# Kernel optimization log

Hardware: AMD Instinct MI355X
Metric: run time of the kernel (lower is better)

## Reference

```python
import jax, jax.numpy as jnp
import numpy as np

B = 16
NS = [2048, 1024, 512, 256]
K = 12
GROUPS = 64
OUT = 1024
EPS = 1e-5


def setup_inputs() -> dict:
    key = jax.random.key(0)
    ks = iter(jax.random.split(key, 40))
    d = {}
    for i, n in enumerate(NS):
        d[f"fs{i}"] = jax.random.normal(next(ks), (B, n, 256), jnp.float32)
        d[f"xs{i}"] = jax.random.normal(next(ks), (B, n, 3), jnp.float32)
        ct = 1024 if i == 0 else 256
        d[f"ft{i}"] = jax.random.normal(next(ks), (B, n, ct), jnp.float32)
        d[f"xt{i}"] = jax.random.normal(next(ks), (B, n, 3), jnp.float32)
    d["Ws"] = jax.random.normal(next(ks), (4, OUT, 256), jnp.float32) * 0.05
    d["bWs"] = jax.random.normal(next(ks), (4, OUT), jnp.float32) * 0.05
    d["gs"] = jax.random.uniform(next(ks), (4, OUT), jnp.float32, 0.5, 1.5)
    d["bes"] = jax.random.normal(next(ks), (4, OUT), jnp.float32) * 0.05
    d["mus"] = jax.random.normal(next(ks), (4, OUT), jnp.float32) * 0.05
    d["vs"] = jax.random.uniform(next(ks), (4, OUT), jnp.float32, 0.5, 1.5)
    d["Wt0"] = jax.random.normal(next(ks), (OUT, 1024), jnp.float32) * 0.02
    d["Wt123"] = jax.random.normal(next(ks), (3, OUT, 256), jnp.float32) * 0.05
    d["bWt"] = jax.random.normal(next(ks), (4, OUT), jnp.float32) * 0.05
    d["gt"] = jax.random.uniform(next(ks), (4, OUT), jnp.float32, 0.5, 1.5)
    d["bet"] = jax.random.normal(next(ks), (4, OUT), jnp.float32) * 0.05
    d["mut"] = jax.random.normal(next(ks), (4, OUT), jnp.float32) * 0.05
    d["vt"] = jax.random.uniform(next(ks), (4, OUT), jnp.float32, 0.5, 1.5)
    return d


def fps(xyz, m):
    # furthest point sampling starting from index 0 (as in pointnet2_utils)
    b, n, _ = xyz.shape
    idxs = jnp.zeros((b, m), jnp.int32)
    d2 = jnp.full((b, n), 1e10, xyz.dtype)
    last = jnp.zeros((b,), jnp.int32)

    def body(i, st):
        idxs, d2, last = st
        lx = jnp.take_along_axis(xyz, last[:, None, None], axis=1)  # [b,1,3]
        d = jnp.sum((xyz - lx) ** 2, axis=-1)  # [b,n]
        d2 = jnp.minimum(d2, d)
        nxt = jnp.argmax(d2, axis=-1).astype(jnp.int32)
        return idxs.at[:, i].set(nxt), d2, nxt

    idxs, _, _ = jax.lax.fori_loop(1, m, body, (idxs, d2, last))
    return idxs


def gather_points(feat, idx):
    # feat [b,n,c], idx [b,...] -> [b,...,c]
    flat = idx.reshape(idx.shape[0], -1)
    out = jnp.take_along_axis(feat, flat[..., None], axis=1)
    return out.reshape(idx.shape + (feat.shape[-1],))


def knn_point(k, xyz, query):
    # squared pairwise distances [b,m,n]; k smallest (== torch.topk largest=False)
    d = (jnp.sum(query ** 2, -1, keepdims=True)
         - 2.0 * jnp.einsum('bmd,bnd->bmn', query, xyz)
         + jnp.sum(xyz ** 2, -1)[:, None, :])
    _, idx = jax.lax.top_k(-d, k)
    return idx.astype(jnp.int32)


def graph_op(grouped, w, b, g, be, mu, v):
    # grouped [B,M,K,C]; kernel-1 Conv1d == channel matmul; eval-mode BN; ReLU; max over K
    x = jnp.einsum('bmkc,oc->bmko', grouped, w) + b
    x = (x - mu) * (g * jax.lax.rsqrt(v + EPS)) + be
    x = jax.nn.relu(x)
    return jnp.max(x, axis=2)  # [B,M,O]


def reference(fs0, xs0, ft0, xt0, fs1, xs1, ft1, xt1, fs2, xs2, ft2, xt2,
              fs3, xs3, ft3, xt3, Ws, bWs, gs, bes, mus, vs,
              Wt0, Wt123, bWt, gt, bet, mut, vt):
    fs_list = [fs0, fs1, fs2, fs3]
    xs_list = [xs0, xs1, xs2, xs3]
    ft_list = [ft0, ft1, ft2, ft3]
    xt_list = [xt0, xt1, xt2, xt3]

    fps_idx = fps(xt_list[-1], GROUPS)              # [B,G]
    new_xyz = gather_points(xt_list[-1], fps_idx)   # [B,G,3]

    out_s, out_t = [], []
    for i in range(4):
        idx_t = knn_point(K, xt_list[i], new_xyz)   # [B,G,K]
        grp_t = gather_points(ft_list[i], idx_t)    # [B,G,K,Ct]
        idx_s = knn_point(K, xs_list[i], new_xyz)
        grp_s = gather_points(fs_list[i], idx_s)    # [B,G,K,256]
        wt = Wt0 if i == 0 else Wt123[i - 1]
        out_s.append(graph_op(grp_s, Ws[i], bWs[i], gs[i], bes[i], mus[i], vs[i]))
        out_t.append(graph_op(grp_t, wt, bWt[i], gt[i], bet[i], mut[i], vt[i]))
    return (tuple(out_s), tuple(out_t))
```

## Files before the change

### kernel.cpp

```cpp
#include <hip/hip_runtime.h>
#include <hip/hip_bf16.h>

#define DEVI __device__ __forceinline__

typedef __attribute__((ext_vector_type(8))) short bf16x8;
typedef __attribute__((ext_vector_type(16))) float f32x16;
typedef __attribute__((ext_vector_type(4))) unsigned int u32x4;
typedef __attribute__((ext_vector_type(4))) float fl4;

DEVI unsigned short f2bf(float f) {
  union { float f; unsigned u; } x; x.f = f;
  unsigned r = (x.u + 0x7fffu + ((x.u >> 16) & 1u)) >> 16;
  return (unsigned short)r;
}

DEVI unsigned cvtpk(float lo, float hi) {
  unsigned r;
  asm("v_cvt_pk_bf16_f32 %0, %1, %2" : "=v"(r) : "v"(lo), "v"(hi));
  return r;
}

DEVI float fadd3(float a, float b, float c) {
  return __fadd_rn(__fadd_rn(a, b), c);
}


__global__ __launch_bounds__(256) void prep_fps_kernel(
    const float* __restrict__ Ws, const float* __restrict__ Wt0,
    const float* __restrict__ Wt123,
    const float* __restrict__ bWs, const float* __restrict__ gs,
    const float* __restrict__ bes, const float* __restrict__ mus,
    const float* __restrict__ vs,
    const float* __restrict__ bWt, const float* __restrict__ gt,
    const float* __restrict__ bet, const float* __restrict__ mut,
    const float* __restrict__ vt, const float* __restrict__ xt3,
    char* __restrict__ wbf, float* __restrict__ bnA, float* __restrict__ bnB,
    float* __restrict__ newxyz) {
  if (blockIdx.x >= 11296u) {
    const int b = blockIdx.x - 11296;
    const int t = threadIdx.x;
    if (t >= 64) return;
    const float* P = xt3 + (size_t)b * 256 * 3;
    float px[4], py[4], pz[4], d2[4];
#pragma unroll
    for (int j = 0; j < 4; ++j) {
      int p = t + 64 * j;
      px[j] = P[p * 3 + 0]; py[j] = P[p * 3 + 1]; pz[j] = P[p * 3 + 2];
      d2[j] = 1e10f;
    }
    float* NX = newxyz + (size_t)b * 64 * 3;
    float cx = __shfl(px[0], 0), cy = __shfl(py[0], 0), cz = __shfl(pz[0], 0);
    if (t == 0) { NX[0] = cx; NX[1] = cy; NX[2] = cz; }
    for (int i = 1; i < 64; ++i) {
      float bv = -1.0f; int bi = 0;
#pragma unroll
      for (int j = 0; j < 4; ++j) {
        float dx = __fsub_rn(px[j], cx), dy = __fsub_rn(py[j], cy),
              dz = __fsub_rn(pz[j], cz);
        float d = fadd3(__fmul_rn(dx, dx), __fmul_rn(dy, dy), __fmul_rn(dz, dz));
        d2[j] = fminf(d2[j], d);
        int p = t + 64 * j;
        if (j == 0) { bv = d2[0]; bi = t; }
        else if (d2[j] > bv) { bv = d2[j]; bi = p; }
      }
#pragma unroll
      for (int off = 32; off >= 1; off >>= 1) {
        float ov = __shfl_xor(bv, off);
        int oi = __shfl_xor(bi, off);
        if (ov > bv || (ov == bv && oi < bi)) { bv = ov; bi = oi; }
      }
      int s = bi;
      int owner = s & 63, slot = s >> 6;
      float sx = slot == 0 ? px[0] : slot == 1 ? px[1] : slot == 2 ? px[2] : px[3];
      float sy = slot == 0 ? py[0] : slot == 1 ? py[1] : slot == 2 ? py[2] : py[3];
      float sz = slot == 0 ? pz[0] : slot == 1 ? pz[1] : slot == 2 ? pz[2] : pz[3];
      cx = __shfl(sx, owner); cy = __shfl(sy, owner); cz = __shfl(sz, owner);
      if (t == 0) { NX[i * 3 + 0] = cx; NX[i * 3 + 1] = cy; NX[i * 3 + 2] = cz; }
    }
    return;
  }
  const unsigned id = blockIdx.x * 256u + threadIdx.x;
  const unsigned WN = 2883584u;
  if (id < WN) {
    float val; unsigned c, o, k, woffE;
    if (id < 1048576u) {
      c = id >> 18; unsigned rem = id & 262143u;
      o = rem >> 8; k = rem & 255u; val = Ws[id]; woffE = c << 18;
    } else if (id < 2097152u) {
      c = 4u; unsigned rem = id - 1048576u;
      o = rem >> 10; k = rem & 1023u; val = Wt0[rem]; woffE = 1048576u;
    } else {
      unsigned rem = id - 2097152u; unsigned cc = rem >> 18;
      c = 5u + cc; unsigned r2 = rem & 262143u;
      o = r2 >> 8; k = r2 & 255u; val = Wt123[rem];
      woffE = 2097152u + (cc << 18);
    }
    unsigned NKT = (c == 4u) ? 16u : 4u;
    unsigned ntile = o >> 8, op = o & 255u, kt = k >> 6, kl = k & 63u;
    unsigned byteoff = (woffE << 1) + ((ntile * NKT + kt) << 15) +
                       (kl >> 3) * 4096u + op * 16u + (kl & 7u) * 2u;
    *(unsigned short*)(wbf + byteoff) = f2bf(val);
  } else {
    unsigned r = id - WN;
    unsigned c = r >> 10, o = r & 1023u;
    float g, bW, mu, v, be;
    if (c < 4u) { g = gs[r]; bW = bWs[r]; mu = mus[r]; v = vs[r]; be = bes[r]; }
    else {
      unsigned r2 = (c - 4u) * 1024u + o;
      g = gt[r2]; bW = bWt[r2]; mu = mut[r2]; v = vt[r2]; be = bet[r2];
    }
    float A = g / sqrtf(v + 1e-5f);
    float B = (bW - mu) * A + be;
    bnA[r] = A; bnB[r] = B;
  }
}

template <int NJ>
DEVI void knn_run(int lane, const float* __restrict__ X, float qx, float qy,
                  float qz, float qq, int* __restrict__ out) {
  float d2[NJ];
#pragma unroll
  for (int j = 0; j < NJ; ++j) {
    int pi = lane + 64 * j;
    float x = X[pi * 3 + 0], y = X[pi * 3 + 1], z = X[pi * 3 + 2];
    float xx = fadd3(__fmul_rn(x, x), __fmul_rn(y, y), __fmul_rn(z, z));
    float dot = fadd3(__fmul_rn(qx, x), __fmul_rn(qy, y), __fmul_rn(qz, z));
    d2[j] = __fadd_rn(__fsub_rn(qq, __fmul_rn(2.0f, dot)), xx);
  }
  for (int kk = 0; kk < 12; ++kk) {
    float bv = d2[0]; int bi = lane;
#pragma unroll
    for (int j = 1; j < NJ; ++j) {
      if (d2[j] < bv) { bv = d2[j]; bi = lane + 64 * j; }
    }
#pragma unroll
    for (int off = 1; off <= 32; off <<= 1) {
      float ov = __shfl_xor(bv, off);
      int oi = __shfl_xor(bi, off);
      if (ov < bv || (ov == bv && oi < bi)) { bv = ov; bi = oi; }
    }
    if (lane == 0) out[kk] = bi;
#pragma unroll
    for (int j = 0; j < NJ; ++j)
      if (bi == lane + 64 * j) d2[j] = 3.4e38f;
  }
}

struct KnnP { const float* xyz[8]; };

__global__ __launch_bounds__(256) void knn_kernel(KnnP p,
                                                  const float* __restrict__ newxyz,
                                                  int* __restrict__ idxbuf) {
  const int q = blockIdx.x * 4 + (threadIdx.x >> 6);
  const int lane = threadIdx.x & 63;
  const int c = q >> 10, b = (q >> 6) & 15, g = q & 63;
  const int n = 2048 >> (c & 3);
  const float* X = p.xyz[c] + (size_t)b * n * 3;
  const float* qp = newxyz + ((size_t)b * 64 + g) * 3;
  float qx = qp[0], qy = qp[1], qz = qp[2];
  float qq = fadd3(__fmul_rn(qx, qx), __fmul_rn(qy, qy), __fmul_rn(qz, qz));
  int* out = idxbuf + (size_t)q * 12;
  switch (c & 3) {
    case 0: knn_run<32>(lane, X, qx, qy, qz, qq, out); break;
    case 1: knn_run<16>(lane, X, qx, qy, qz, qq, out); break;
    case 2: knn_run<8>(lane, X, qx, qy, qz, qq, out); break;
    default: knn_run<4>(lane, X, qx, qy, qz, qq, out); break;
  }
}

struct GImgP {
  const float* feat[8];
  int n[8];
  int K[8];
  int NKT[8];
  unsigned goffB[8];
  unsigned base[9];
};

__global__ __launch_bounds__(256) void gather_img_kernel(
    GImgP p, const int* __restrict__ idxbuf, char* __restrict__ grouped) {
  const unsigned blk = blockIdx.x;
  int c = 0;
#pragma unroll
  for (int j = 1; j < 8; ++j) if (blk >= p.base[j]) c = j;
  const unsigned local = blk - p.base[c];
  const int NKT = p.NKT[c];
  const int mtile = local / NKT;
  const int kt = local - mtile * NKT;
  const int row = threadIdx.x;
  const int gl = row >> 4, kslot = row & 15;
  const int ke = (kslot < 12) ? kslot : 0;
  const int group = mtile * 16 + gl;
  const int b = group >> 6;
  const int pidx = idxbuf[(size_t)c * 12288 + group * 12 + ke];
  const int K = p.K[c];
  const float* src = p.feat[c] + ((size_t)b * p.n[c] + pidx) * K + kt * 64;
  char* dst = grouped + p.goffB[c] + ((size_t)(mtile * NKT + kt)) * 32768u +
              row * 16;
#pragma unroll
  for (int s = 0; s < 8; ++s) {
    fl4 v0 = *reinterpret_cast<const fl4*>(src + s * 8);
    fl4 v1 = *reinterpret_cast<const fl4*>(src + s * 8 + 4);
    u32x4 w;
    w[0] = cvtpk(v0[0], v0[1]);
    w[1] = cvtpk(v0[2], v0[3]);
    w[2] = cvtpk(v1[0], v1[1]);
    w[3] = cvtpk(v1[2], v1[3]);
    *reinterpret_cast<u32x4*>(dst + s * 4096) = w;
  }
}

struct GemmPR {
  unsigned goff[8]; unsigned woff[8]; unsigned outoff[8];
  unsigned bnoff[8]; int K[8];
};

#define GLOAD_LDS16(gsrc, ldsdst)                                              \
  __builtin_amdgcn_global_load_lds(                                            \
      (const __attribute__((address_space(1))) void*)(gsrc),                   \
      (__attribute__((address_space(3))) void*)(ldsdst), 16, 0, 0)

__global__ __launch_bounds__(512, 2) void gemm_pers_kernel(
    const char* __restrict__ grouped, const char* __restrict__ wbf,
    const float* __restrict__ bnA, const float* __restrict__ bnB,
    float* __restrict__ out, GemmPR p) {
  extern __shared__ char smem[];
  const int bid = blockIdx.x;
  const int xcd = bid & 7, slot = bid >> 3;
  const int rem = (xcd << 5) | slot;
  const int mtile = rem >> 2, ntile = rem & 3;
  const int tid = threadIdx.x;
  const int lane = tid & 63, wid = tid >> 6;
  const int wr = wid >> 2, wc = wid & 3;

  const int aoff = (lane >> 5) * 4096 + (wr * 128 + (lane & 31)) * 16;
  const int boff = (lane >> 5) * 4096 + (wc * 64 + (lane & 31)) * 16;

  f32x16 acc[4][2];
#pragma unroll
  for (int j = 0; j < 4; ++j)
#pragma unroll
    for (int nn = 0; nn < 2; ++nn)
#pragma unroll
      for (int e = 0; e < 16; ++e) acc[j][nn][e] = 0.f;

  auto stageA = [&](int par, const char* src) {
    char* dst = smem + par * 65536;
#pragma unroll
    for (int it = 0; it < 4; ++it)
      GLOAD_LDS16(src + (it * 512 + tid) * 16, dst + (it * 512 + wid * 64) * 16);
  };
  auto stageB = [&](int par, const char* src) {
    char* dst = smem + par * 65536 + 32768;
#pragma unroll
    for (int it = 0; it < 4; ++it)
      GLOAD_LDS16(src + (it * 512 + tid) * 16, dst + (it * 512 + wid * 64) * 16);
  };

  int nkt = p.K[0] >> 6;
  const char* Ac = grouped + p.goff[0] + (size_t)mtile * nkt * 32768;
  const char* Bc = wbf + p.woff[0] + (size_t)ntile * nkt * 32768;

  stageA(0, Ac);
  stageB(0, Bc);
  __syncthreads();

  int gs = 0;
  for (int zi = 0; zi < 8; ++zi) {
    nkt = p.K[zi] >> 6;
    const char* An = nullptr;
    const char* Bn = nullptr;
    if (zi < 7) {
      int nktN = p.K[zi + 1] >> 6;
      An = grouped + p.goff[zi + 1] + (size_t)mtile * nktN * 32768;
      Bn = wbf + p.woff[zi + 1] + (size_t)ntile * nktN * 32768;
    }
    for (int kt = 0; kt < nkt; ++kt, ++gs) {
      const int par = gs & 1;
      const char* As = smem + par * 65536;
      const char* Bs = As + 32768;

      if (gs + 1 < 44) {
        int k1 = kt + 1;
        const char* sA, * sB;
        if (k1 < nkt) { sA = Ac + (size_t)k1 * 32768; sB = Bc + (size_t)k1 * 32768; }
        else { sA = An; sB = Bn; }
        stageA(par ^ 1, sA);
        stageB(par ^ 1, sB);
      }

      bf16x8 bv[4][2], af[2][4];
#pragma unroll
      for (int ks = 0; ks < 4; ++ks)
#pragma unroll
        for (int nn = 0; nn < 2; ++nn)
          bv[ks][nn] = *reinterpret_cast<const bf16x8*>(
              Bs + ks * 8192 + nn * 512 + boff);
#pragma unroll
      for (int ks2 = 0; ks2 < 2; ++ks2)
#pragma unroll
        for (int j = 0; j < 4; ++j)
          af[ks2][j] = *reinterpret_cast<const bf16x8*>(
              As + ks2 * 8192 + j * 512 + aoff);
#pragma unroll
      for (int ks2 = 0; ks2 < 2; ++ks2)
#pragma unroll
        for (int j = 0; j < 4; ++j)
#pragma unroll
          for (int nn = 0; nn < 2; ++nn)
            acc[j][nn] = __builtin_amdgcn_mfma_f32_32x32x16_bf16(
                af[ks2][j], bv[ks2][nn], acc[j][nn], 0, 0, 0);
#pragma unroll
      for (int ks2 = 0; ks2 < 2; ++ks2)
#pragma unroll
        for (int j = 0; j < 4; ++j)
          af[ks2][j] = *reinterpret_cast<const bf16x8*>(
              As + 16384 + ks2 * 8192 + j * 512 + aoff);
#pragma unroll
      for (int ks2 = 0; ks2 < 2; ++ks2)
#pragma unroll
        for (int j = 0; j < 4; ++j)
#pragma unroll
          for (int nn = 0; nn < 2; ++nn)
            acc[j][nn] = __builtin_amdgcn_mfma_f32_32x32x16_bf16(
                af[ks2][j], bv[2 + ks2][nn], acc[j][nn], 0, 0, 0);

      __syncthreads();
    }

    const float* bA = bnA + p.bnoff[zi];
    const float* bB = bnB + p.bnoff[zi];
    float* O = out + (size_t)p.outoff[zi];
#pragma unroll
    for (int nn = 0; nn < 2; ++nn) {
      int colb = ntile * 256 + wc * 64 + nn * 32 + (lane & 31);
      float sA = bA[colb], sB = bB[colb];
#pragma unroll
      for (int j = 0; j < 4; ++j) {
#pragma unroll
        for (int h = 0; h < 2; ++h) {
          float v = acc[j][nn][8 * h];
#pragma unroll
          for (int e = 1; e < 8; ++e) v = fmaxf(v, acc[j][nn][8 * h + e]);
          v = fmaxf(v, __shfl_xor(v, 32));
          if (lane < 32) {
            int grp = mtile * 16 + wr * 8 + j * 2 + h;
            float val = fmaf(v, sA, sB);
            O[(size_t)grp * 1024 + colb] = fmaxf(val, 0.f);
          }
        }
      }
    }
#pragma unroll
    for (int j = 0; j < 4; ++j)
#pragma unroll
      for (int nn = 0; nn < 2; ++nn)
#pragma unroll
        for (int e = 0; e < 16; ++e) acc[j][nn][e] = 0.f;
    Ac = An;
    Bc = Bn;
  }
}

extern "C" void kernel_launch(void* const* d_in, const int* in_sizes, int n_in,
                              void* d_out, int out_size, void* d_ws,
                              size_t ws_size, hipStream_t stream) {
  (void)in_sizes; (void)n_in; (void)out_size; (void)ws_size;
  const float *fs[4], *xs[4], *ft[4], *xt[4];
  for (int i = 0; i < 4; ++i) {
    fs[i] = (const float*)d_in[4 * i + 0];
    xs[i] = (const float*)d_in[4 * i + 1];
    ft[i] = (const float*)d_in[4 * i + 2];
    xt[i] = (const float*)d_in[4 * i + 3];
  }
  const float* Ws = (const float*)d_in[16];
  const float* bWs = (const float*)d_in[17];
  const float* gs = (const float*)d_in[18];
  const float* bes = (const float*)d_in[19];
  const float* mus = (const float*)d_in[20];
  const float* vs = (const float*)d_in[21];
  const float* Wt0 = (const float*)d_in[22];
  const float* Wt123 = (const float*)d_in[23];
  const float* bWt = (const float*)d_in[24];
  const float* gt = (const float*)d_in[25];
  const float* bet = (const float*)d_in[26];
  const float* mut = (const float*)d_in[27];
  const float* vt = (const float*)d_in[28];

  char* ws = (char*)d_ws;
  float* newxyz = (float*)(ws + 0);
  int* idxbuf = (int*)(ws + 16384);
  float* bnA = (float*)(ws + 409600);
  float* bnB = (float*)(ws + 442368);
  char* wbf = ws + 475136;
  char* grouped = ws + 6242304;

  static const int NSarr[4] = {2048, 1024, 512, 256};
  const unsigned goffB[8] = {0u,        8388608u,  16777216u, 25165824u,
                             33554432u, 67108864u, 75497472u, 83886080u};
  const unsigned woffB[8] = {0u,       524288u,  1048576u, 1572864u,
                             2097152u, 4194304u, 4718592u, 5242880u};

  prep_fps_kernel<<<11312, 256, 0, stream>>>(Ws, Wt0, Wt123, bWs, gs, bes, mus,
                                             vs, bWt, gt, bet, mut, vt, xt[3],
                                             wbf, bnA, bnB, newxyz);

  KnnP kp;
  for (int i = 0; i < 4; ++i) {
    kp.xyz[i] = xs[i];
    kp.xyz[4 + i] = xt[i];
  }
  knn_kernel<<<2048, 256, 0, stream>>>(kp, newxyz, idxbuf);

  GImgP gp;
  unsigned cum = 0;
  for (int c = 0; c < 8; ++c) {
    int scale = c & 3;
    gp.feat[c] = (c < 4) ? fs[scale] : ft[scale];
    gp.n[c] = NSarr[scale];
    gp.K[c] = (c == 4) ? 1024 : 256;
    gp.NKT[c] = (c == 4) ? 16 : 4;
    gp.goffB[c] = goffB[c];
    gp.base[c] = cum;
    cum += 64u * (unsigned)gp.NKT[c];
  }
  gp.base[8] = cum;
  gather_img_kernel<<<cum, 256, 0, stream>>>(gp, idxbuf, grouped);

  static const int co[8] = {0, 1, 2, 3, 5, 6, 7, 4};
  GemmPR mp;
  for (int zi = 0; zi < 8; ++zi) {
    int c = co[zi];
    mp.goff[zi] = goffB[c]; mp.woff[zi] = woffB[c];
    mp.outoff[zi] = (unsigned)c * 1048576u;
    mp.bnoff[zi] = (unsigned)c * 1024u;
    mp.K[zi] = (c == 4) ? 1024 : 256;
  }
  (void)hipFuncSetAttribute((const void*)gemm_pers_kernel,
                            hipFuncAttributeMaxDynamicSharedMemorySize, 131072);
  gemm_pers_kernel<<<256, 512, 131072, stream>>>(grouped, wbf, bnA, bnB,
                                                 (float*)d_out, mp);
}
```

Baseline: 218.4 us.

## Fuse KNN with feature gather and use 16 waves in persistent GEMM

Merges the KNN and gather kernels into one kernel per 16-group tile. Neighbour indices stay in shared memory instead of taking a round trip through a global index buffer and a separate launch, and padding rows are no longer written. The persistent GEMM moves to 1024 threads per block, so each wave owns half as many rows and uses fewer accumulators. The epilogue now skips the padded rows when taking the max. The cost is less KNN parallelism, since each wave now handles four queries in sequence, plus register pressure at 1024 threads and possible stale data in the unwritten padding slots.

```diff
diff --git a/kernel.cpp b/kernel.cpp
--- a/kernel.cpp
+++ b/kernel.cpp
@@ -146,67 +146,63 @@
   }
 }
 
-struct KnnP { const float* xyz[8]; };
-
-__global__ __launch_bounds__(256) void knn_kernel(KnnP p,
-                                                  const float* __restrict__ newxyz,
-                                                  int* __restrict__ idxbuf) {
-  const int q = blockIdx.x * 4 + (threadIdx.x >> 6);
-  const int lane = threadIdx.x & 63;
-  const int c = q >> 10, b = (q >> 6) & 15, g = q & 63;
-  const int n = 2048 >> (c & 3);
+struct KGP {
+  const float* feat[8];
+  const float* xyz[8];
+  unsigned goffB[8];
+};
+
+__global__ __launch_bounds__(256) void knn_gather_kernel(
+    KGP p, const float* __restrict__ newxyz, char* __restrict__ grouped) {
+  const int blk = blockIdx.x;
+  int c, mtile;
+  if (blk < 64) { c = 4; mtile = blk; }
+  else { int r = blk - 64; int ci = r >> 6; c = (ci < 4) ? ci : ci + 1; mtile = r & 63; }
+  const int scale = c & 3;
+  const int n = 2048 >> scale;
+  const int K = (c == 4) ? 1024 : 256;
+  const int NKT = K >> 6;
+  const int b = mtile >> 2;
+
+  __shared__ int idxs[16][12];
+  const int wid = threadIdx.x >> 6, lane = threadIdx.x & 63;
   const float* X = p.xyz[c] + (size_t)b * n * 3;
-  const float* qp = newxyz + ((size_t)b * 64 + g) * 3;
-  float qx = qp[0], qy = qp[1], qz = qp[2];
-  float qq = fadd3(__fmul_rn(qx, qx), __fmul_rn(qy, qy), __fmul_rn(qz, qz));
-  int* out = idxbuf + (size_t)q * 12;
-  switch (c & 3) {
-    case 0: knn_run<32>(lane, X, qx, qy, qz, qq, out); break;
-    case 1: knn_run<16>(lane, X, qx, qy, qz, qq, out); break;
-    case 2: knn_run<8>(lane, X, qx, qy, qz, qq, out); break;
-    default: knn_run<4>(lane, X, qx, qy, qz, qq, out); break;
-  }
-}
-
-struct GImgP {
-  const float* feat[8];
-  int n[8];
-  int K[8];
-  int NKT[8];
-  unsigned goffB[8];
-  unsigned base[9];
-};
-
-__global__ __launch_bounds__(256) void gather_img_kernel(
-    GImgP p, const int* __restrict__ idxbuf, char* __restrict__ grouped) {
-  const unsigned blk = blockIdx.x;
-  int c = 0;
-#pragma unroll
-  for (int j = 1; j < 8; ++j) if (blk >= p.base[j]) c = j;
-  const unsigned local = blk - p.base[c];
-  const int NKT = p.NKT[c];
-  const int mtile = local / NKT;
-  const int kt = local - mtile * NKT;
+
+  for (int qi = 0; qi < 4; ++qi) {
+    const int gl = wid * 4 + qi;
+    const int g = (mtile & 3) * 16 + gl;
+    const float* qp = newxyz + ((size_t)b * 64 + g) * 3;
+    float qx = qp[0], qy = qp[1], qz = qp[2];
+    float qq = fadd3(__fmul_rn(qx, qx), __fmul_rn(qy, qy), __fmul_rn(qz, qz));
+    switch (scale) {
+      case 0: knn_run<32>(lane, X, qx, qy, qz, qq, idxs[gl]); break;
+      case 1: knn_run<16>(lane, X, qx, qy, qz, qq, idxs[gl]); break;
+      case 2: knn_run<8>(lane, X, qx, qy, qz, qq, idxs[gl]); break;
+      default: knn_run<4>(lane, X, qx, qy, qz, qq, idxs[gl]); break;
+    }
+  }
+  __syncthreads();
+
   const int row = threadIdx.x;
   const int gl = row >> 4, kslot = row & 15;
-  const int ke = (kslot < 12) ? kslot : 0;
-  const int group = mtile * 16 + gl;
-  const int b = group >> 6;
-  const int pidx = idxbuf[(size_t)c * 12288 + group * 12 + ke];
-  const int K = p.K[c];
-  const float* src = p.feat[c] + ((size_t)b * p.n[c] + pidx) * K + kt * 64;
-  char* dst = grouped + p.goffB[c] + ((size_t)(mtile * NKT + kt)) * 32768u +
-              row * 16;
-#pragma unroll
-  for (int s = 0; s < 8; ++s) {
-    fl4 v0 = *reinterpret_cast<const fl4*>(src + s * 8);
-    fl4 v1 = *reinterpret_cast<const fl4*>(src + s * 8 + 4);
-    u32x4 w;
-    w[0] = cvtpk(v0[0], v0[1]);
-    w[1] = cvtpk(v0[2], v0[3]);
-    w[2] = cvtpk(v1[0], v1[1]);
-    w[3] = cvtpk(v1[2], v1[3]);
-    *reinterpret_cast<u32x4*>(dst + s * 4096) = w;
+  if (kslot >= 12) return;
+  const int pidx = idxs[gl][kslot];
+  const float* rowbase = p.feat[c] + ((size_t)b * n + pidx) * K;
+  char* dstbase = grouped + p.goffB[c] + (size_t)mtile * NKT * 32768u + row * 16;
+  for (int kt = 0; kt < NKT; ++kt) {
+    const float* src = rowbase + kt * 64;
+    char* dst = dstbase + (size_t)kt * 32768u;
+#pragma unroll
+    for (int s = 0; s < 8; ++s) {
+      fl4 v0 = *reinterpret_cast<const fl4*>(src + s * 8);
+      fl4 v1 = *reinterpret_cast<const fl4*>(src + s * 8 + 4);
+      u32x4 w;
+      w[0] = cvtpk(v0[0], v0[1]);
+      w[1] = cvtpk(v0[2], v0[3]);
+      w[2] = cvtpk(v1[0], v1[1]);
+      w[3] = cvtpk(v1[2], v1[3]);
+      *reinterpret_cast<u32x4*>(dst + s * 4096) = w;
+    }
   }
 }
 
@@ -220,7 +216,7 @@
       (const __attribute__((address_space(1))) void*)(gsrc),                   \
       (__attribute__((address_space(3))) void*)(ldsdst), 16, 0, 0)
 
-__global__ __launch_bounds__(512, 2) void gemm_pers_kernel(
+__global__ __launch_bounds__(1024, 4) void gemm_pers_kernel(
     const char* __restrict__ grouped, const char* __restrict__ wbf,
     const float* __restrict__ bnA, const float* __restrict__ bnB,
     float* __restrict__ out, GemmPR p) {
@@ -233,12 +229,12 @@
   const int lane = tid & 63, wid = tid >> 6;
   const int wr = wid >> 2, wc = wid & 3;
 
-  const int aoff = (lane >> 5) * 4096 + (wr * 128 + (lane & 31)) * 16;
+  const int aoff = (lane >> 5) * 4096 + (wr * 64 + (lane & 31)) * 16;
   const int boff = (lane >> 5) * 4096 + (wc * 64 + (lane & 31)) * 16;
 
-  f32x16 acc[4][2];
-#pragma unroll
-  for (int j = 0; j < 4; ++j)
+  f32x16 acc[2][2];
+#pragma unroll
+  for (int j = 0; j < 2; ++j)
 #pragma unroll
     for (int nn = 0; nn < 2; ++nn)
 #pragma unroll
@@ -247,14 +243,14 @@
   auto stageA = [&](int par, const char* src) {
     char* dst = smem + par * 65536;
 #pragma unroll
-    for (int it = 0; it < 4; ++it)
-      GLOAD_LDS16(src + (it * 512 + tid) * 16, dst + (it * 512 + wid * 64) * 16);
+    for (int it = 0; it < 2; ++it)
+      GLOAD_LDS16(src + (it * 1024 + tid) * 16, dst + (it * 1024 + wid * 64) * 16);
   };
   auto stageB = [&](int par, const char* src) {
     char* dst = smem + par * 65536 + 32768;
 #pragma unroll
-    for (int it = 0; it < 4; ++it)
-      GLOAD_LDS16(src + (it * 512 + tid) * 16, dst + (it * 512 + wid * 64) * 16);
+    for (int it = 0; it < 2; ++it)
+      GLOAD_LDS16(src + (it * 1024 + tid) * 16, dst + (it * 1024 + wid * 64) * 16);
   };
 
   int nkt = p.K[0] >> 6;
@@ -289,7 +285,7 @@
         stageB(par ^ 1, sB);
       }
 
-      bf16x8 bv[4][2], af[2][4];
+      bf16x8 bv[4][2], af[4][2];
 #pragma unroll
       for (int ks = 0; ks < 4; ++ks)
 #pragma unroll
@@ -297,33 +293,19 @@
           bv[ks][nn] = *reinterpret_cast<const bf16x8*>(
               Bs + ks * 8192 + nn * 512 + boff);
 #pragma unroll
-      for (int ks2 = 0; ks2 < 2; ++ks2)
-#pragma unroll
-        for (int j = 0; j < 4; ++j)
-          af[ks2][j] = *reinterpret_cast<const bf16x8*>(
-              As + ks2 * 8192 + j * 512 + aoff);
-#pragma unroll
-      for (int ks2 = 0; ks2 < 2; ++ks2)
-#pragma unroll
-        for (int j = 0; j < 4; ++j)
+      for (int ks = 0; ks < 4; ++ks)
+#pragma unroll
+        for (int j = 0; j < 2; ++j)
+          af[ks][j] = *reinterpret_cast<const bf16x8*>(
+              As + ks * 8192 + j * 512 + aoff);
+#pragma unroll
+      for (int ks = 0; ks < 4; ++ks)
+#pragma unroll
+        for (int j = 0; j < 2; ++j)
 #pragma unroll
           for (int nn = 0; nn < 2; ++nn)
             acc[j][nn] = __builtin_amdgcn_mfma_f32_32x32x16_bf16(
-                af[ks2][j], bv[ks2][nn], acc[j][nn], 0, 0, 0);
-#pragma unroll
-      for (int ks2 = 0; ks2 < 2; ++ks2)
-#pragma unroll
-        for (int j = 0; j < 4; ++j)
-          af[ks2][j] = *reinterpret_cast<const bf16x8*>(
-              As + 16384 + ks2 * 8192 + j * 512 + aoff);
-#pragma unroll
-      for (int ks2 = 0; ks2 < 2; ++ks2)
-#pragma unroll
-        for (int j = 0; j < 4; ++j)
-#pragma unroll
-          for (int nn = 0; nn < 2; ++nn)
-            acc[j][nn] = __builtin_amdgcn_mfma_f32_32x32x16_bf16(
-                af[ks2][j], bv[2 + ks2][nn], acc[j][nn], 0, 0, 0);
+                af[ks][j], bv[ks][nn], acc[j][nn], 0, 0, 0);
 
       __syncthreads();
     }
@@ -331,20 +313,23 @@
     const float* bA = bnA + p.bnoff[zi];
     const float* bB = bnB + p.bnoff[zi];
     float* O = out + (size_t)p.outoff[zi];
+    const bool hi0 = (lane < 32);
 #pragma unroll
     for (int nn = 0; nn < 2; ++nn) {
       int colb = ntile * 256 + wc * 64 + nn * 32 + (lane & 31);
       float sA = bA[colb], sB = bB[colb];
 #pragma unroll
-      for (int j = 0; j < 4; ++j) {
+      for (int j = 0; j < 2; ++j) {
 #pragma unroll
         for (int h = 0; h < 2; ++h) {
-          float v = acc[j][nn][8 * h];
-#pragma unroll
-          for (int e = 1; e < 8; ++e) v = fmaxf(v, acc[j][nn][8 * h + e]);
+          float v = fmaxf(fmaxf(acc[j][nn][8 * h + 0], acc[j][nn][8 * h + 1]),
+                          fmaxf(acc[j][nn][8 * h + 2], acc[j][nn][8 * h + 3]));
+          float v2 = fmaxf(fmaxf(acc[j][nn][8 * h + 4], acc[j][nn][8 * h + 5]),
+                           fmaxf(acc[j][nn][8 * h + 6], acc[j][nn][8 * h + 7]));
+          if (hi0) v = fmaxf(v, v2);
           v = fmaxf(v, __shfl_xor(v, 32));
-          if (lane < 32) {
-            int grp = mtile * 16 + wr * 8 + j * 2 + h;
+          if (hi0) {
+            int grp = mtile * 16 + wr * 4 + j * 2 + h;
             float val = fmaf(v, sA, sB);
             O[(size_t)grp * 1024 + colb] = fmaxf(val, 0.f);
           }
@@ -352,7 +337,7 @@
       }
     }
 #pragma unroll
-    for (int j = 0; j < 4; ++j)
+    for (int j = 0; j < 2; ++j)
 #pragma unroll
       for (int nn = 0; nn < 2; ++nn)
 #pragma unroll
@@ -389,13 +374,11 @@
 
   char* ws = (char*)d_ws;
   float* newxyz = (float*)(ws + 0);
-  int* idxbuf = (int*)(ws + 16384);
   float* bnA = (float*)(ws + 409600);
   float* bnB = (float*)(ws + 442368);
   char* wbf = ws + 475136;
   char* grouped = ws + 6242304;
 
-  static const int NSarr[4] = {2048, 1024, 512, 256};
   const unsigned goffB[8] = {0u,        8388608u,  16777216u, 25165824u,
                              33554432u, 67108864u, 75497472u, 83886080u};
   const unsigned woffB[8] = {0u,       524288u,  1048576u, 1572864u,
@@ -405,27 +388,14 @@
                                              vs, bWt, gt, bet, mut, vt, xt[3],
                                              wbf, bnA, bnB, newxyz);
 
-  KnnP kp;
-  for (int i = 0; i < 4; ++i) {
-    kp.xyz[i] = xs[i];
-    kp.xyz[4 + i] = xt[i];
-  }
-  knn_kernel<<<2048, 256, 0, stream>>>(kp, newxyz, idxbuf);
-
-  GImgP gp;
-  unsigned cum = 0;
+  KGP kg;
   for (int c = 0; c < 8; ++c) {
     int scale = c & 3;
-    gp.feat[c] = (c < 4) ? fs[scale] : ft[scale];
-    gp.n[c] = NSarr[scale];
-    gp.K[c] = (c == 4) ? 1024 : 256;
-    gp.NKT[c] = (c == 4) ? 16 : 4;
-    gp.goffB[c] = goffB[c];
-    gp.base[c] = cum;
-    cum += 64u * (unsigned)gp.NKT[c];
-  }
-  gp.base[8] = cum;
-  gather_img_kernel<<<cum, 256, 0, stream>>>(gp, idxbuf, grouped);
+    kg.feat[c] = (c < 4) ? fs[scale] : ft[scale];
+    kg.xyz[c] = (c < 4) ? xs[scale] : xt[scale];
+    kg.goffB[c] = goffB[c];
+  }
+  knn_gather_kernel<<<512, 256, 0, stream>>>(kg, newxyz, grouped);
 
   static const int co[8] = {0, 1, 2, 3, 5, 6, 7, 4};
   GemmPR mp;
@@ -438,6 +408,6 @@
   }
   (void)hipFuncSetAttribute((const void*)gemm_pers_kernel,
                             hipFuncAttributeMaxDynamicSharedMemorySize, 131072);
-  gemm_pers_kernel<<<256, 512, 131072, stream>>>(grouped, wbf, bnA, bnB,
-                                                 (float*)d_out, mp);
-}
+  gemm_pers_kernel<<<256, 1024, 131072, stream>>>(grouped, wbf, bnA, bnB,
+                                                  (float*)d_out, mp);
+}
```

Measured after the change: 251.3 us. 15.0% more time.

## Double GEMM block to 16 waves with smaller per-wave tiles; skip padded gather rows

Applied to the files above, without the earlier changes.

The persistent GEMM now launches 1024 threads per block instead of 512. Each wave owns a 64x64 output tile with a 2x2 accumulator array instead of 128x64, and the A/B staging loops take half as many iterations each. The epilogue masks out the padded K slots (12-15), so the gather kernel can return early for those rows instead of duplicating slot 0, which saves loads and writes. The cost is that each wave does less MFMA work per LDS fragment read, and the aggressive launch bound (1024, 4) may constrain registers; the padded rows of the grouped buffer are now left uninitialized.

```diff
diff --git a/kernel.cpp b/kernel.cpp
--- a/kernel.cpp
+++ b/kernel.cpp
@@ -189,10 +189,10 @@
   const int kt = local - mtile * NKT;
   const int row = threadIdx.x;
   const int gl = row >> 4, kslot = row & 15;
-  const int ke = (kslot < 12) ? kslot : 0;
+  if (kslot >= 12) return;
   const int group = mtile * 16 + gl;
   const int b = group >> 6;
-  const int pidx = idxbuf[(size_t)c * 12288 + group * 12 + ke];
+  const int pidx = idxbuf[(size_t)c * 12288 + group * 12 + kslot];
   const int K = p.K[c];
   const float* src = p.feat[c] + ((size_t)b * p.n[c] + pidx) * K + kt * 64;
   char* dst = grouped + p.goffB[c] + ((size_t)(mtile * NKT + kt)) * 32768u +
@@ -220,7 +220,7 @@
       (const __attribute__((address_space(1))) void*)(gsrc),                   \
       (__attribute__((address_space(3))) void*)(ldsdst), 16, 0, 0)
 
-__global__ __launch_bounds__(512, 2) void gemm_pers_kernel(
+__global__ __launch_bounds__(1024, 4) void gemm_pers_kernel(
     const char* __restrict__ grouped, const char* __restrict__ wbf,
     const float* __restrict__ bnA, const float* __restrict__ bnB,
     float* __restrict__ out, GemmPR p) {
@@ -233,12 +233,12 @@
   const int lane = tid & 63, wid = tid >> 6;
   const int wr = wid >> 2, wc = wid & 3;
 
-  const int aoff = (lane >> 5) * 4096 + (wr * 128 + (lane & 31)) * 16;
+  const int aoff = (lane >> 5) * 4096 + (wr * 64 + (lane & 31)) * 16;
   const int boff = (lane >> 5) * 4096 + (wc * 64 + (lane & 31)) * 16;
 
-  f32x16 acc[4][2];
-#pragma unroll
-  for (int j = 0; j < 4; ++j)
+  f32x16 acc[2][2];
+#pragma unroll
+  for (int j = 0; j < 2; ++j)
 #pragma unroll
     for (int nn = 0; nn < 2; ++nn)
 #pragma unroll
@@ -247,14 +247,14 @@
   auto stageA = [&](int par, const char* src) {
     char* dst = smem + par * 65536;
 #pragma unroll
-    for (int it = 0; it < 4; ++it)
-      GLOAD_LDS16(src + (it * 512 + tid) * 16, dst + (it * 512 + wid * 64) * 16);
+    for (int it = 0; it < 2; ++it)
+      GLOAD_LDS16(src + (it * 1024 + tid) * 16, dst + (it * 1024 + wid * 64) * 16);
   };
   auto stageB = [&](int par, const char* src) {
     char* dst = smem + par * 65536 + 32768;
 #pragma unroll
-    for (int it = 0; it < 4; ++it)
-      GLOAD_LDS16(src + (it * 512 + tid) * 16, dst + (it * 512 + wid * 64) * 16);
+    for (int it = 0; it < 2; ++it)
+      GLOAD_LDS16(src + (it * 1024 + tid) * 16, dst + (it * 1024 + wid * 64) * 16);
   };
 
   int nkt = p.K[0] >> 6;
@@ -289,7 +289,7 @@
         stageB(par ^ 1, sB);
       }
 
-      bf16x8 bv[4][2], af[2][4];
+      bf16x8 bv[4][2], af[4][2];
 #pragma unroll
       for (int ks = 0; ks < 4; ++ks)
 #pragma unroll
@@ -297,33 +297,19 @@
           bv[ks][nn] = *reinterpret_cast<const bf16x8*>(
               Bs + ks * 8192 + nn * 512 + boff);
 #pragma unroll
-      for (int ks2 = 0; ks2 < 2; ++ks2)
-#pragma unroll
-        for (int j = 0; j < 4; ++j)
-          af[ks2][j] = *reinterpret_cast<const bf16x8*>(
-              As + ks2 * 8192 + j * 512 + aoff);
-#pragma unroll
-      for (int ks2 = 0; ks2 < 2; ++ks2)
-#pragma unroll
-        for (int j = 0; j < 4; ++j)
+      for (int ks = 0; ks < 4; ++ks)
+#pragma unroll
+        for (int j = 0; j < 2; ++j)
+          af[ks][j] = *reinterpret_cast<const bf16x8*>(
+              As + ks * 8192 + j * 512 + aoff);
+#pragma unroll
+      for (int ks = 0; ks < 4; ++ks)
+#pragma unroll
+        for (int j = 0; j < 2; ++j)
 #pragma unroll
           for (int nn = 0; nn < 2; ++nn)
             acc[j][nn] = __builtin_amdgcn_mfma_f32_32x32x16_bf16(
-                af[ks2][j], bv[ks2][nn], acc[j][nn], 0, 0, 0);
-#pragma unroll
-      for (int ks2 = 0; ks2 < 2; ++ks2)
-#pragma unroll
-        for (int j = 0; j < 4; ++j)
-          af[ks2][j] = *reinterpret_cast<const bf16x8*>(
-              As + 16384 + ks2 * 8192 + j * 512 + aoff);
-#pragma unroll
-      for (int ks2 = 0; ks2 < 2; ++ks2)
-#pragma unroll
-        for (int j = 0; j < 4; ++j)
-#pragma unroll
-          for (int nn = 0; nn < 2; ++nn)
-            acc[j][nn] = __builtin_amdgcn_mfma_f32_32x32x16_bf16(
-                af[ks2][j], bv[2 + ks2][nn], acc[j][nn], 0, 0, 0);
+                af[ks][j], bv[ks][nn], acc[j][nn], 0, 0, 0);
 
       __syncthreads();
     }
@@ -331,20 +317,23 @@
     const float* bA = bnA + p.bnoff[zi];
     const float* bB = bnB + p.bnoff[zi];
     float* O = out + (size_t)p.outoff[zi];
+    const bool hi0 = (lane < 32);
 #pragma unroll
     for (int nn = 0; nn < 2; ++nn) {
       int colb = ntile * 256 + wc * 64 + nn * 32 + (lane & 31);
       float sA = bA[colb], sB = bB[colb];
 #pragma unroll
-      for (int j = 0; j < 4; ++j) {
+      for (int j = 0; j < 2; ++j) {
 #pragma unroll
         for (int h = 0; h < 2; ++h) {
-          float v = acc[j][nn][8 * h];
-#pragma unroll
-          for (int e = 1; e < 8; ++e) v = fmaxf(v, acc[j][nn][8 * h + e]);
+          float v = fmaxf(fmaxf(acc[j][nn][8 * h + 0], acc[j][nn][8 * h + 1]),
+                          fmaxf(acc[j][nn][8 * h + 2], acc[j][nn][8 * h + 3]));
+          float v2 = fmaxf(fmaxf(acc[j][nn][8 * h + 4], acc[j][nn][8 * h + 5]),
+                           fmaxf(acc[j][nn][8 * h + 6], acc[j][nn][8 * h + 7]));
+          if (hi0) v = fmaxf(v, v2);
           v = fmaxf(v, __shfl_xor(v, 32));
-          if (lane < 32) {
-            int grp = mtile * 16 + wr * 8 + j * 2 + h;
+          if (hi0) {
+            int grp = mtile * 16 + wr * 4 + j * 2 + h;
             float val = fmaf(v, sA, sB);
             O[(size_t)grp * 1024 + colb] = fmaxf(val, 0.f);
           }
@@ -352,7 +341,7 @@
       }
     }
 #pragma unroll
-    for (int j = 0; j < 4; ++j)
+    for (int j = 0; j < 2; ++j)
 #pragma unroll
       for (int nn = 0; nn < 2; ++nn)
 #pragma unroll
@@ -438,6 +427,6 @@
   }
   (void)hipFuncSetAttribute((const void*)gemm_pers_kernel,
                             hipFuncAttributeMaxDynamicSharedMemorySize, 131072);
-  gemm_pers_kernel<<<256, 512, 131072, stream>>>(grouped, wbf, bnA, bnB,
-                                                 (float*)d_out, mp);
-}
+  gemm_pers_kernel<<<256, 1024, 131072, stream>>>(grouped, wbf, bnA, bnB,
+                                                  (float*)d_out, mp);
+}
```

After: 215.4 us. Within noise of the previous version (-1.4%).
